# Kernel tuning notes

Measured on AMD Instinct MI355X. Metric: run time of the kernel, lower is better.

The kernel has to match this reference:

```python
import jax, jax.numpy as jnp
import numpy as np

N_NODES = 100000
N_EDGES = 1600000
D_IN = 128
D_HID = 128
D_OUT = 128
ORIG = 90000


def setup_inputs() -> dict:
    key = jax.random.key(0)
    ks = jax.random.split(key, 8)
    x = jax.random.normal(ks[0], (N_NODES, D_IN), dtype=jnp.float32)
    edge_index = jax.random.randint(ks[1], (2, N_EDGES), 0, N_NODES, dtype=jnp.int64)
    # Glorot-ish scaled weights; PyG SAGEConv: lin_l (with bias) on aggregated, lin_r (no bias) on root
    s1 = 1.0 / np.sqrt(D_IN)
    s2 = 1.0 / np.sqrt(D_HID)
    Wl1 = jax.random.normal(ks[2], (D_IN, D_HID), dtype=jnp.float32) * s1
    bl1 = jnp.zeros((D_HID,), dtype=jnp.float32)
    Wr1 = jax.random.normal(ks[3], (D_IN, D_HID), dtype=jnp.float32) * s1
    Wl2 = jax.random.normal(ks[4], (D_HID, D_OUT), dtype=jnp.float32) * s2
    bl2 = jnp.zeros((D_OUT,), dtype=jnp.float32)
    Wr2 = jax.random.normal(ks[5], (D_HID, D_OUT), dtype=jnp.float32) * s2
    return {"x": x, "edge_index": edge_index, "original_size": ORIG,
            "Wl1": Wl1, "bl1": bl1, "Wr1": Wr1,
            "Wl2": Wl2, "bl2": bl2, "Wr2": Wr2}


def _sage_conv(x, src, dst, Wl, bl, Wr):
    # PyG SAGEConv (aggr='mean'): out = lin_l(mean_{j in N(i)} x_j) + lin_r(x_i)
    n = x.shape[0]
    msgs = x[src]                                            # [E, d] gather
    ssum = jax.ops.segment_sum(msgs, dst, num_segments=n)    # [N, d]
    cnt = jax.ops.segment_sum(jnp.ones((src.shape[0],), dtype=x.dtype), dst,
                              num_segments=n)                # [N]
    mean = ssum / jnp.maximum(cnt, 1.0)[:, None]             # 0 for isolated nodes
    return mean @ Wl + bl + x @ Wr


def reference(x, edge_index, original_size, Wl1, bl1, Wr1, Wl2, bl2, Wr2):
    src, dst = edge_index[0], edge_index[1]
    h = _sage_conv(x, src, dst, Wl1, bl1, Wr1)
    h = _sage_conv(h, src, dst, Wl2, bl2, Wr2)
    return h[:original_size]
```

## Files before the change

### kernel.cpp

```cpp
#include <hip/hip_runtime.h>

#define NN 100000
#define DD 128

typedef __attribute__((ext_vector_type(8))) short bf16x8;
typedef __attribute__((ext_vector_type(4))) float f32x4;
typedef __attribute__((ext_vector_type(2))) float f32x2;

__device__ __forceinline__ float bf2f(unsigned short u) {
    union { unsigned int i; float f; } v;
    v.i = ((unsigned int)u) << 16;
    return v.f;
}

__device__ __forceinline__ unsigned short f2bf(float f) {
    union { float f; unsigned int i; } v;
    v.f = f;
    unsigned int x = v.i;
    return (unsigned short)((x + 0x7FFFu + ((x >> 16) & 1u)) >> 16);
}

__device__ __forceinline__ float2 load2(const float* p, int i2) {
    return ((const float2*)p)[i2];
}

__device__ __forceinline__ f32x2 cvt2(unsigned int u) {
    union { unsigned int i; float f; } lo, hi;
    lo.i = u << 16;
    hi.i = u & 0xffff0000u;
    return (f32x2){lo.f, hi.f};
}

__device__ __forceinline__ bf16x8 load8_bf(const unsigned short* p) {
    return *((const bf16x8*)p);
}
__device__ __forceinline__ bf16x8 load8_bf(const float* p) {
    float4 a = ((const float4*)p)[0];
    float4 b = ((const float4*)p)[1];
    bf16x8 r;
    r[0] = (short)f2bf(a.x); r[1] = (short)f2bf(a.y);
    r[2] = (short)f2bf(a.z); r[3] = (short)f2bf(a.w);
    r[4] = (short)f2bf(b.x); r[5] = (short)f2bf(b.y);
    r[6] = (short)f2bf(b.z); r[7] = (short)f2bf(b.w);
    return r;
}


#define PCH 16
#define NBUKMAX 512
#define CAP 12288

__global__ __launch_bounds__(256) void hist_buckets(
    const int* __restrict__ ei, int E, int* __restrict__ bcnt, int nbuk) {
    __shared__ int is64_s;
    __shared__ int hl[NBUKMAX];
    int tid = threadIdx.x;
    for (int i = tid; i < nbuk; i += 256) hl[i] = 0;
    if (tid < 64) {
        int ok = (ei[2 * tid + 1] == 0);
        int all = __all(ok);
        if (tid == 0) is64_s = all;
    }
    __syncthreads();
    int is64 = is64_s;
    int e0 = blockIdx.x * (256 * PCH) + tid;
#pragma unroll
    for (int c = 0; c < PCH; c++) {
        int e = e0 + c * 256;
        if (e < E) {
            int d = is64 ? ei[2 * (E + e)] : ei[E + e];
            atomicAdd(&hl[d >> 8], 1);
        }
    }
    __syncthreads();
    for (int i = tid; i < nbuk; i += 256) {
        int v = hl[i];
        if (v) atomicAdd(&bcnt[i], v);
    }
}

__global__ void scan_buckets(const int* __restrict__ bcnt, int nbuk,
                             int* __restrict__ boff, int* __restrict__ offN, int E) {
    __shared__ int wsum[8];
    int tid = threadIdx.x;
    int lane = tid & 63, wid = tid >> 6;
    int v = (tid < nbuk) ? bcnt[tid] : 0;
    int s = v;
#pragma unroll
    for (int dl = 1; dl < 64; dl <<= 1) {
        int t = __shfl_up(s, dl, 64);
        if (lane >= dl) s += t;
    }
    if (lane == 63) wsum[wid] = s;
    __syncthreads();
    int w = 0;
#pragma unroll
    for (int i = 0; i < 8; i++) w += (i < wid) ? wsum[i] : 0;
    if (tid < nbuk) boff[tid] = w + s - v;
    if (tid == nbuk - 1) boff[nbuk] = w + s;
    if (tid == 0) offN[0] = E;
}

__global__ __launch_bounds__(256) void partition_edges(
    const int* __restrict__ ei, int E, const int* __restrict__ boff,
    int* __restrict__ bcur, unsigned long long* __restrict__ pairs, int nbuk) {
    __shared__ int is64_s;
    __shared__ int cntb[NBUKMAX];
    __shared__ int baseb[NBUKMAX];
    __shared__ int boffb[NBUKMAX];
    int tid = threadIdx.x;
    for (int i = tid; i < nbuk; i += 256) {
        cntb[i] = 0;
        boffb[i] = boff[i];
    }
    if (tid < 64) {
        int ok = (ei[2 * tid + 1] == 0);
        int all = __all(ok);
        if (tid == 0) is64_s = all;
    }
    __syncthreads();
    int is64 = is64_s;
    int e0 = blockIdx.x * (256 * PCH) + tid;

    int dv[PCH], sv[PCH], bl[PCH];
    bool va[PCH];
#pragma unroll
    for (int c = 0; c < PCH; c++) {
        int e = e0 + c * 256;
        va[c] = (e < E);
        dv[c] = va[c] ? (is64 ? ei[2 * (E + e)] : ei[E + e]) : 0;
        sv[c] = va[c] ? (is64 ? ei[2 * e] : ei[e]) : 0;
        bl[c] = 0;
    }
#pragma unroll
    for (int c = 0; c < PCH; c++) {
        if (va[c]) {
            int b = dv[c] >> 8;
            int l = atomicAdd(&cntb[b], 1);
            bl[c] = (b << 16) | l;
        }
    }
    __syncthreads();
    for (int i = tid; i < nbuk; i += 256) {
        int cb = cntb[i];
        baseb[i] = cb ? atomicAdd(&bcur[i], cb) : 0;
    }
    __syncthreads();
#pragma unroll
    for (int c = 0; c < PCH; c++) {
        if (va[c]) {
            int b = bl[c] >> 16, l = bl[c] & 0xffff;
            pairs[(size_t)(boffb[b] + baseb[b] + l)] =
                ((unsigned long long)(unsigned int)dv[c] << 32) | (unsigned int)sv[c];
        }
    }
}

__global__ __launch_bounds__(256) void build_csr(
    const unsigned long long* __restrict__ pairs, const int* __restrict__ boff,
    int* __restrict__ off, int* __restrict__ csr, int* __restrict__ cur, int N) {
    int b = blockIdx.x;
    int lo = b << 8;
    if (lo >= N) return;
    int hi = min(lo + 256, N);
    int nn = hi - lo;
    int base = boff[b];
    int pcount = boff[b + 1] - base;

    __shared__ int cnt_l[256];
    __shared__ int start_l[256];
    __shared__ int cur_l[256];
    __shared__ int wsum[4];
    __shared__ int lds_csr[CAP];

    int tid = threadIdx.x;
    cnt_l[tid] = 0;
    __syncthreads();

    for (int i = tid; i < pcount; i += 256) {
        int d = (int)(pairs[base + i] >> 32);
        atomicAdd(&cnt_l[d - lo], 1);
    }
    __syncthreads();

    int v = cnt_l[tid];
    int s = v;
    int lane = tid & 63, wid = tid >> 6;
#pragma unroll
    for (int dl = 1; dl < 64; dl <<= 1) {
        int t = __shfl_up(s, dl, 64);
        if (lane >= dl) s += t;
    }
    if (lane == 63) wsum[wid] = s;
    __syncthreads();
    int w = 0;
#pragma unroll
    for (int i = 0; i < 4; i++) w += (i < wid) ? wsum[i] : 0;
    int excl = w + s - v;
    start_l[tid] = excl;
    cur_l[tid] = excl;
    if (tid < nn) off[lo + tid] = base + excl;
    __syncthreads();

    if (pcount <= CAP) {
        for (int i = tid; i < pcount; i += 256) {
            unsigned long long p = pairs[base + i];
            int d = (int)(p >> 32) - lo;
            int pos = atomicAdd(&cur_l[d], 1);
            lds_csr[pos] = (int)(p & 0xffffffffu);
        }
        __syncthreads();
        for (int i = tid; i < pcount; i += 256) csr[base + i] = lds_csr[i];
    } else {
        for (int i = tid; i < pcount; i += 256) {
            unsigned long long p = pairs[base + i];
            int dg = (int)(p >> 32);
            int q = atomicAdd(&cur[dg], 1);
            csr[base + start_l[dg - lo] + q] = (int)(p & 0xffffffffu);
        }
    }
}

__global__ void cast_bf16(const float* __restrict__ in, unsigned short* __restrict__ out,
                          int n4) {
    int i = blockIdx.x * blockDim.x + threadIdx.x;
    if (i >= n4) return;
    float4 v = ((const float4*)in)[i];
    ushort4 o;
    o.x = f2bf(v.x); o.y = f2bf(v.y); o.z = f2bf(v.z); o.w = f2bf(v.w);
    ((ushort4*)out)[i] = o;
}

__global__ void prep_weights(const float* __restrict__ Wl1, const float* __restrict__ Wr1,
                             const float* __restrict__ Wl2, const float* __restrict__ Wr2,
                             unsigned short* __restrict__ Wt1, unsigned short* __restrict__ Wt2) {
    __shared__ float t[32][33];
    int which = blockIdx.x >> 4;
    const float* W = (which == 0) ? Wl1 : (which == 1) ? Wr1 : (which == 2) ? Wl2 : Wr2;
    unsigned short* Wt = (which < 2) ? Wt1 : Wt2;
    int koff = (which & 1) * 128;
    int b = blockIdx.x & 15;
    int bx = b & 3, by = b >> 2;
    int c = threadIdx.x & 31, r8 = threadIdx.x >> 5;
#pragma unroll
    for (int i = 0; i < 4; i++) {
        int r = r8 + i * 8;
        t[r][c] = W[(by * 32 + r) * 128 + bx * 32 + c];
    }
    __syncthreads();
#pragma unroll
    for (int i = 0; i < 4; i++) {
        int r = r8 + i * 8;
        Wt[(bx * 32 + r) * 256 + koff + by * 32 + c] = f2bf(t[c][r]);
    }
}

#define ACC8(u) do { \
    acc[0] += cvt2((u).x); acc[1] += cvt2((u).y); \
    acc[2] += cvt2((u).z); acc[3] += cvt2((u).w); } while (0)

__global__ __launch_bounds__(256) void aggregate_bf(
    const unsigned short* __restrict__ feat,
    const int* __restrict__ off, const int* __restrict__ csr,
    unsigned short* __restrict__ mean, int N, const int* __restrict__ limp) {
    int lim = limp ? min(N, limp[0]) : N;
    int node = blockIdx.x * 4 + (threadIdx.x >> 6);
    if (node >= lim) return;
    int lane = threadIdx.x & 63;
    int e = lane >> 4, q = lane & 15;
    int s0 = off[node], s1 = off[node + 1];

    f32x2 acc[4];
#pragma unroll
    for (int t = 0; t < 4; t++) acc[t] = (f32x2){0.f, 0.f};

    for (int c0 = s0; c0 < s1; c0 += 64) {
        int cdeg = min(64, s1 - c0);
        int cr = (lane < cdeg) ? csr[c0 + lane] : 0;
        int nb = (cdeg + 15) >> 4;

        uint4 C0 = make_uint4(0, 0, 0, 0), C1 = C0, C2 = C0, C3 = C0;
        {
            int i0 = e, i1 = e + 4, i2 = e + 8, i3 = e + 12;
            int t0 = __shfl(cr, i0, 64), t1 = __shfl(cr, i1, 64),
                t2 = __shfl(cr, i2, 64), t3 = __shfl(cr, i3, 64);
            if (i0 < cdeg) C0 = *((const uint4*)(feat + (size_t)t0 * 128 + q * 8));
            if (i1 < cdeg) C1 = *((const uint4*)(feat + (size_t)t1 * 128 + q * 8));
            if (i2 < cdeg) C2 = *((const uint4*)(feat + (size_t)t2 * 128 + q * 8));
            if (i3 < cdeg) C3 = *((const uint4*)(feat + (size_t)t3 * 128 + q * 8));
        }
        for (int b = 1; b < nb; b++) {
            int i0 = b * 16 + e, i1 = i0 + 4, i2 = i0 + 8, i3 = i0 + 12;
            int t0 = __shfl(cr, i0, 64), t1 = __shfl(cr, i1, 64),
                t2 = __shfl(cr, i2, 64), t3 = __shfl(cr, i3, 64);
            uint4 N0 = make_uint4(0, 0, 0, 0), N1 = N0, N2 = N0, N3 = N0;
            if (i0 < cdeg) N0 = *((const uint4*)(feat + (size_t)t0 * 128 + q * 8));
            if (i1 < cdeg) N1 = *((const uint4*)(feat + (size_t)t1 * 128 + q * 8));
            if (i2 < cdeg) N2 = *((const uint4*)(feat + (size_t)t2 * 128 + q * 8));
            if (i3 < cdeg) N3 = *((const uint4*)(feat + (size_t)t3 * 128 + q * 8));
            ACC8(C0); ACC8(C1); ACC8(C2); ACC8(C3);
            C0 = N0; C1 = N1; C2 = N2; C3 = N3;
        }
        ACC8(C0); ACC8(C1); ACC8(C2); ACC8(C3);
    }

#pragma unroll
    for (int t = 0; t < 4; t++) {
        union { f32x2 v; double d; } a, b;
        a.v = acc[t];
        b.d = __shfl_xor(a.d, 16, 64); a.v += b.v;
        b.d = __shfl_xor(a.d, 32, 64); a.v += b.v;
        acc[t] = a.v;
    }

    int deg = s1 - s0;
    float inv = (deg > 0) ? (1.0f / (float)deg) : 0.0f;
    if (e == 0) {
        bf16x8 o;
#pragma unroll
        for (int t = 0; t < 4; t++) {
            o[2 * t]     = (short)f2bf(acc[t].x * inv);
            o[2 * t + 1] = (short)f2bf(acc[t].y * inv);
        }
        *((bf16x8*)(mean + (size_t)node * 128 + q * 8)) = o;
    }
}

__global__ void aggregate_f32(const float* __restrict__ feat,
                              const int* __restrict__ off, const int* __restrict__ csr,
                              unsigned short* __restrict__ mean, int N) {
    int node = blockIdx.x * (blockDim.x >> 6) + (threadIdx.x >> 6);
    if (node >= N) return;
    int lane = threadIdx.x & 63;
    int s0 = off[node], s1 = off[node + 1];
    float ax = 0.f, ay = 0.f;
    for (int j = s0; j < s1; j++) {
        int s = csr[j];
        float2 v = load2(feat, s * 64 + lane);
        ax += v.x; ay += v.y;
    }
    float inv = (s1 > s0) ? (1.0f / (float)(s1 - s0)) : 0.0f;
    unsigned int p = (unsigned int)f2bf(ax * inv) | ((unsigned int)f2bf(ay * inv) << 16);
    ((unsigned int*)mean)[node * 64 + lane] = p;
}

template <typename TA2, typename TO>
__global__ __launch_bounds__(256) void gemm_mfma(
    const unsigned short* __restrict__ A1, const TA2* __restrict__ A2,
    const unsigned short* __restrict__ Wt, const float* __restrict__ bias,
    TO* __restrict__ out, int Arows, int Nlimit, const int* __restrict__ origp) {
    int lim = Nlimit;
    if (origp) lim = min(lim, origp[0]);
    int n0 = blockIdx.x * 64;
    if (n0 >= lim) return;

    int tid = threadIdx.x;
    int lane = tid & 63;
    int wid = tid >> 6;
    int wm = wid >> 1, wn = wid & 1;
    int qd = lane >> 4, l16 = lane & 15;

    int r0 = min(n0 + wm * 32 + l16, Arows - 1);
    int r1 = min(n0 + wm * 32 + 16 + l16, Arows - 1);

    f32x4 acc[2][4];
#pragma unroll
    for (int a = 0; a < 2; a++)
#pragma unroll
        for (int b = 0; b < 4; b++) acc[a][b] = (f32x4){0.f, 0.f, 0.f, 0.f};

#pragma unroll
    for (int ks = 0; ks < 8; ks++) {
        int kb = (ks & 3) * 32;
        bf16x8 a0, a1;
        if (ks < 4) {
            a0 = load8_bf(A1 + (size_t)r0 * 128 + kb + qd * 8);
            a1 = load8_bf(A1 + (size_t)r1 * 128 + kb + qd * 8);
        } else {
            a0 = load8_bf(A2 + (size_t)r0 * 128 + kb + qd * 8);
            a1 = load8_bf(A2 + (size_t)r1 * 128 + kb + qd * 8);
        }
#pragma unroll
        for (int tn = 0; tn < 4; tn++) {
            int f = wn * 64 + tn * 16 + l16;
            bf16x8 bfrag = *((const bf16x8*)(Wt + f * 256 + ks * 32 + qd * 8));
            acc[0][tn] = __builtin_amdgcn_mfma_f32_16x16x32_bf16(a0, bfrag, acc[0][tn], 0, 0, 0);
            acc[1][tn] = __builtin_amdgcn_mfma_f32_16x16x32_bf16(a1, bfrag, acc[1][tn], 0, 0, 0);
        }
    }

#pragma unroll
    for (int tn = 0; tn < 4; tn++) {
        int f = wn * 64 + tn * 16 + l16;
        float bv = bias[f];
#pragma unroll
        for (int tm = 0; tm < 2; tm++) {
#pragma unroll
            for (int r = 0; r < 4; r++) {
                int n = n0 + wm * 32 + tm * 16 + qd * 4 + r;
                if (n < lim) {
                    float val = acc[tm][tn][r] + bv;
                    if constexpr (__is_same(TO, float))
                        out[n * 128 + f] = val;
                    else
                        out[n * 128 + f] = f2bf(val);
                }
            }
        }
    }
}

extern "C" void kernel_launch(void* const* d_in, const int* in_sizes, int n_in,
                              void* d_out, int out_size, void* d_ws, size_t ws_size,
                              hipStream_t stream) {
    const float* x   = (const float*)d_in[0];
    const int*   ei  = (const int*)d_in[1];
    const int*   org = (const int*)d_in[2];
    const float* Wl1 = (const float*)d_in[3];
    const float* bl1 = (const float*)d_in[4];
    const float* Wr1 = (const float*)d_in[5];
    const float* Wl2 = (const float*)d_in[6];
    const float* bl2 = (const float*)d_in[7];
    const float* Wr2 = (const float*)d_in[8];
    float* out = (float*)d_out;

    const int N = in_sizes[0] / DD;
    const int E = in_sizes[1] / 2;

    size_t szFeat = (size_t)N * DD * 2;
    size_t szBase = 2 * szFeat
                  + 2 * 65536
                  + (size_t)N * 4 + 4096
                  + (size_t)(N + 1) * 4
                  + 4096
                  + (size_t)E * 4;
    bool big = ws_size >= szBase + szFeat + 4096;

    char* ws = (char*)d_ws;
    unsigned short* mean = (unsigned short*)ws;  ws += szFeat;
    unsigned short* h    = (unsigned short*)ws;  ws += szFeat;
    unsigned short* xb   = nullptr;
    if (big) { xb = (unsigned short*)ws; ws += szFeat; }
    unsigned short* Wt1 = (unsigned short*)ws;  ws += 65536;
    unsigned short* Wt2 = (unsigned short*)ws;  ws += 65536;
    int* cur  = (int*)ws;  ws += (size_t)N * 4;
    int* bcnt = (int*)ws;  ws += 2048;
    int* bcur = (int*)ws;  ws += 2048;
    int* off  = (int*)ws;  ws += (size_t)(N + 1) * 4;
    int* boff = (int*)ws;  ws += 4096;
    int* csr  = (int*)ws;

    unsigned long long* pairs = (unsigned long long*)mean;

    int nbuk = (N + 255) >> 8;
    int edgeGrid = (E + 256 * PCH - 1) / (256 * PCH);

    hipMemsetAsync(cur, 0, (size_t)N * 4 + 4096, stream);
    hist_buckets<<<edgeGrid, 256, 0, stream>>>(ei, E, bcnt, nbuk);
    scan_buckets<<<1, 512, 0, stream>>>(bcnt, nbuk, boff, off + N, E);
    partition_edges<<<edgeGrid, 256, 0, stream>>>(ei, E, boff, bcur, pairs, nbuk);
    build_csr<<<nbuk, 256, 0, stream>>>(pairs, boff, off, csr, cur, N);

    prep_weights<<<64, 256, 0, stream>>>(Wl1, Wr1, Wl2, Wr2, Wt1, Wt2);

    int aggGrid  = (N + 3) / 4;
    int gemmGrid = (N + 63) / 64;

    if (big) {
        cast_bf16<<<(N * DD / 4 + 255) / 256, 256, 0, stream>>>(x, xb, N * DD / 4);
        aggregate_bf<<<aggGrid, 256, 0, stream>>>(xb, off, csr, mean, N, nullptr);
        gemm_mfma<unsigned short, unsigned short><<<gemmGrid, 256, 0, stream>>>(
            mean, xb, Wt1, bl1, h, N, N, nullptr);
    } else {
        aggregate_f32<<<aggGrid, 256, 0, stream>>>(x, off, csr, mean, N);
        gemm_mfma<float, unsigned short><<<gemmGrid, 256, 0, stream>>>(
            mean, x, Wt1, bl1, h, N, N, nullptr);
    }
    aggregate_bf<<<aggGrid, 256, 0, stream>>>(h, off, csr, mean, N, org);
    gemm_mfma<unsigned short, float><<<gemmGrid, 256, 0, stream>>>(
        mean, h, Wt2, bl2, out, N, N, org);
}
```

Measured before the change: 360.7 us.

## Process four nodes per wavefront in bf16 aggregation with cross-node gather prefetch

Each wavefront in aggregate_bf now handles four consecutive nodes instead of one. It loads their offsets with one coalesced read and preloads the first 64 CSR indices for each node up front. The first neighbour batch of the next node is prefetched while the current node's tail batch is accumulated, so loads from different nodes overlap and per-node launch and latency overhead is amortised. The cost is higher register pressure from the extra prefetch buffers. Nodes with more than 64 neighbours fall back to an unpipelined loop.

```diff
diff --git a/kernel.cpp b/kernel.cpp
--- a/kernel.cpp
+++ b/kernel.cpp
@@ -259,70 +259,95 @@
     acc[0] += cvt2((u).x); acc[1] += cvt2((u).y); \
     acc[2] += cvt2((u).z); acc[3] += cvt2((u).w); } while (0)
 
+#define GATH4(D0, D1, D2, D3, crg, cdeg, b) do { \
+    int i0 = (b) * 16 + e, i1 = i0 + 4, i2 = i0 + 8, i3 = i0 + 12; \
+    int t0 = __shfl((crg), i0, 64), t1 = __shfl((crg), i1, 64), \
+        t2 = __shfl((crg), i2, 64), t3 = __shfl((crg), i3, 64); \
+    D0 = make_uint4(0, 0, 0, 0); D1 = D0; D2 = D0; D3 = D0; \
+    if (i0 < (cdeg)) D0 = *((const uint4*)(feat + (size_t)t0 * 128 + q * 8)); \
+    if (i1 < (cdeg)) D1 = *((const uint4*)(feat + (size_t)t1 * 128 + q * 8)); \
+    if (i2 < (cdeg)) D2 = *((const uint4*)(feat + (size_t)t2 * 128 + q * 8)); \
+    if (i3 < (cdeg)) D3 = *((const uint4*)(feat + (size_t)t3 * 128 + q * 8)); \
+} while (0)
+
 __global__ __launch_bounds__(256) void aggregate_bf(
     const unsigned short* __restrict__ feat,
     const int* __restrict__ off, const int* __restrict__ csr,
     unsigned short* __restrict__ mean, int N, const int* __restrict__ limp) {
     int lim = limp ? min(N, limp[0]) : N;
-    int node = blockIdx.x * 4 + (threadIdx.x >> 6);
-    if (node >= lim) return;
+    int nb0 = (blockIdx.x * 4 + (int)(threadIdx.x >> 6)) * 4;
+    if (nb0 >= lim) return;
     int lane = threadIdx.x & 63;
     int e = lane >> 4, q = lane & 15;
-    int s0 = off[node], s1 = off[node + 1];
+
+    int offv = off[min(nb0 + min(lane, 4), N)];
+    int s0g[4], dg[4], cr[4];
+#pragma unroll
+    for (int g = 0; g < 4; g++) {
+        int s0 = __shfl(offv, g, 64);
+        int s1 = __shfl(offv, g + 1, 64);
+        bool valid = (nb0 + g) < lim;
+        s0g[g] = s0;
+        dg[g] = valid ? (s1 - s0) : 0;
+        int nd = min(dg[g], 64);
+        cr[g] = (lane < nd) ? csr[s0 + lane] : 0;
+    }
 
     f32x2 acc[4];
-#pragma unroll
-    for (int t = 0; t < 4; t++) acc[t] = (f32x2){0.f, 0.f};
-
-    for (int c0 = s0; c0 < s1; c0 += 64) {
-        int cdeg = min(64, s1 - c0);
-        int cr = (lane < cdeg) ? csr[c0 + lane] : 0;
-        int nb = (cdeg + 15) >> 4;
-
-        uint4 C0 = make_uint4(0, 0, 0, 0), C1 = C0, C2 = C0, C3 = C0;
-        {
-            int i0 = e, i1 = e + 4, i2 = e + 8, i3 = e + 12;
-            int t0 = __shfl(cr, i0, 64), t1 = __shfl(cr, i1, 64),
-                t2 = __shfl(cr, i2, 64), t3 = __shfl(cr, i3, 64);
-            if (i0 < cdeg) C0 = *((const uint4*)(feat + (size_t)t0 * 128 + q * 8));
-            if (i1 < cdeg) C1 = *((const uint4*)(feat + (size_t)t1 * 128 + q * 8));
-            if (i2 < cdeg) C2 = *((const uint4*)(feat + (size_t)t2 * 128 + q * 8));
-            if (i3 < cdeg) C3 = *((const uint4*)(feat + (size_t)t3 * 128 + q * 8));
-        }
-        for (int b = 1; b < nb; b++) {
-            int i0 = b * 16 + e, i1 = i0 + 4, i2 = i0 + 8, i3 = i0 + 12;
-            int t0 = __shfl(cr, i0, 64), t1 = __shfl(cr, i1, 64),
-                t2 = __shfl(cr, i2, 64), t3 = __shfl(cr, i3, 64);
-            uint4 N0 = make_uint4(0, 0, 0, 0), N1 = N0, N2 = N0, N3 = N0;
-            if (i0 < cdeg) N0 = *((const uint4*)(feat + (size_t)t0 * 128 + q * 8));
-            if (i1 < cdeg) N1 = *((const uint4*)(feat + (size_t)t1 * 128 + q * 8));
-            if (i2 < cdeg) N2 = *((const uint4*)(feat + (size_t)t2 * 128 + q * 8));
-            if (i3 < cdeg) N3 = *((const uint4*)(feat + (size_t)t3 * 128 + q * 8));
+    uint4 C0, C1, C2, C3, P0, P1, P2, P3;
+    {
+        int cd0 = min(dg[0], 64);
+        GATH4(C0, C1, C2, C3, cr[0], cd0, 0);
+    }
+
+#pragma unroll
+    for (int g = 0; g < 4; g++) {
+        int cdeg = min(dg[g], 64);
+        int nbt = (cdeg + 15) >> 4;
+#pragma unroll
+        for (int t = 0; t < 4; t++) acc[t] = (f32x2){0.f, 0.f};
+        for (int b = 1; b < nbt; b++) {
+            GATH4(P0, P1, P2, P3, cr[g], cdeg, b);
             ACC8(C0); ACC8(C1); ACC8(C2); ACC8(C3);
-            C0 = N0; C1 = N1; C2 = N2; C3 = N3;
+            C0 = P0; C1 = P1; C2 = P2; C3 = P3;
+        }
+        if (g < 3) {
+            int cdn = min(dg[g + 1], 64);
+            GATH4(P0, P1, P2, P3, cr[g + 1], cdn, 0);
         }
         ACC8(C0); ACC8(C1); ACC8(C2); ACC8(C3);
-    }
-
-#pragma unroll
-    for (int t = 0; t < 4; t++) {
-        union { f32x2 v; double d; } a, b;
-        a.v = acc[t];
-        b.d = __shfl_xor(a.d, 16, 64); a.v += b.v;
-        b.d = __shfl_xor(a.d, 32, 64); a.v += b.v;
-        acc[t] = a.v;
-    }
-
-    int deg = s1 - s0;
-    float inv = (deg > 0) ? (1.0f / (float)deg) : 0.0f;
-    if (e == 0) {
-        bf16x8 o;
+
+        int s1e = s0g[g] + dg[g];
+        for (int c0 = s0g[g] + 64; c0 < s1e; c0 += 64) {
+            int cd2 = min(64, s1e - c0);
+            int cr2 = (lane < cd2) ? csr[c0 + lane] : 0;
+            int nb2 = (cd2 + 15) >> 4;
+            for (int b = 0; b < nb2; b++) {
+                uint4 E0, E1, E2, E3;
+                GATH4(E0, E1, E2, E3, cr2, cd2, b);
+                ACC8(E0); ACC8(E1); ACC8(E2); ACC8(E3);
+            }
+        }
+
 #pragma unroll
         for (int t = 0; t < 4; t++) {
-            o[2 * t]     = (short)f2bf(acc[t].x * inv);
-            o[2 * t + 1] = (short)f2bf(acc[t].y * inv);
-        }
-        *((bf16x8*)(mean + (size_t)node * 128 + q * 8)) = o;
+            union { f32x2 v; double d; } a, bb;
+            a.v = acc[t];
+            bb.d = __shfl_xor(a.d, 16, 64); a.v += bb.v;
+            bb.d = __shfl_xor(a.d, 32, 64); a.v += bb.v;
+            acc[t] = a.v;
+        }
+        float inv = (dg[g] > 0) ? (1.0f / (float)dg[g]) : 0.0f;
+        if (e == 0 && (nb0 + g) < lim) {
+            bf16x8 o;
+#pragma unroll
+            for (int t = 0; t < 4; t++) {
+                o[2 * t]     = (short)f2bf(acc[t].x * inv);
+                o[2 * t + 1] = (short)f2bf(acc[t].y * inv);
+            }
+            *((bf16x8*)(mean + (size_t)(nb0 + g) * 128 + q * 8)) = o;
+        }
+        if (g < 3) { C0 = P0; C1 = P1; C2 = P2; C3 = P3; }
     }
 }
 
@@ -463,7 +488,8 @@
 
     prep_weights<<<64, 256, 0, stream>>>(Wl1, Wr1, Wl2, Wr2, Wt1, Wt2);
 
-    int aggGrid  = (N + 3) / 4;
+    int aggGrid  = (N + 15) / 16;
+    int aggGridF = (N + 3) / 4;
     int gemmGrid = (N + 63) / 64;
 
     if (big) {
@@ -472,7 +498,7 @@
         gemm_mfma<unsigned short, unsigned short><<<gemmGrid, 256, 0, stream>>>(
             mean, xb, Wt1, bl1, h, N, N, nullptr);
     } else {
-        aggregate_f32<<<aggGrid, 256, 0, stream>>>(x, off, csr, mean, N);
+        aggregate_f32<<<aggGridF, 256, 0, stream>>>(x, off, csr, mean, N);
         gemm_mfma<float, unsigned short><<<gemmGrid, 256, 0, stream>>>(
             mean, x, Wt1, bl1, h, N, N, nullptr);
     }
```

After: 360.8 us. No clear change (+0.0%).
